# Performance work log

Hardware: AMD Instinct MI355X
Metric: run time of the kernel (lower is better)

## Reference

```python
import jax, jax.numpy as jnp
import numpy as np

B, S_NEW, D = 8, 16, 2048
H, HD = 16, 128
PAST = 4096


def setup_inputs() -> dict:
    key = jax.random.key(0)
    ks = jax.random.split(key, 8)
    w = 0.02
    return {
        "x": jax.random.normal(ks[0], (B, S_NEW, D), jnp.float32),
        "k_cache": jax.random.normal(ks[1], (B, H, PAST, HD), jnp.float32),
        "v_cache": jax.random.normal(ks[2], (B, H, PAST, HD), jnp.float32),
        "Wq": jax.random.normal(ks[3], (D, D), jnp.float32) * w,
        "bq": jnp.zeros((D,), jnp.float32),
        "Wk": jax.random.normal(ks[4], (D, D), jnp.float32) * w,
        "bk": jnp.zeros((D,), jnp.float32),
        "Wv": jax.random.normal(ks[5], (D, D), jnp.float32) * w,
        "bv": jnp.zeros((D,), jnp.float32),
        "Wo": jax.random.normal(ks[6], (D, D), jnp.float32) * w,
        "bo": jnp.zeros((D,), jnp.float32),
    }


def reference(x, k_cache, v_cache, Wq, bq, Wk, bk, Wv, bv, Wo, bo):
    B_, S_new, D_ = x.shape
    H_ = H
    hd = D_ // H_
    scale = hd ** (-0.5)

    def proj(W, b):
        # [B,S,D] -> [B,H,S,hd]
        return (x @ W + b).reshape(B_, S_new, H_, hd).transpose(0, 2, 1, 3)

    q = proj(Wq, bq)
    k_new = proj(Wk, bk)
    v_new = proj(Wv, bv)

    # cache.append + get_full_kv: concat along sequence axis
    k = jnp.concatenate([k_cache, k_new], axis=2)  # [B,H,S_full,hd]
    v = jnp.concatenate([v_cache, v_new], axis=2)
    S_full = k.shape[2]
    past = S_full - S_new

    scores = jnp.einsum("bhqd,bhkd->bhqk", q, k) * scale  # [B,H,S_new,S_full]

    # triu(ones(S_new,S_full), diagonal=past+1): mask key j when j - i > past
    i = jnp.arange(S_new)[:, None]
    j = jnp.arange(S_full)[None, :]
    mask = (j - i) > past  # [S_new, S_full] bool
    scores = jnp.where(mask[None, None, :, :], -jnp.inf, scores)

    attn = jax.nn.softmax(scores, axis=-1)  # dropout is identity in eval
    out = jnp.einsum("bhqk,bhkd->bhqd", attn, v)  # [B,H,S_new,hd]
    out = out.transpose(0, 2, 1, 3).reshape(B_, S_new, D_)
    return out @ Wo + bo
```

## Files before the change

kernel.cpp:

```cpp
#include <hip/hip_runtime.h>
#include <stdint.h>

#define B_    8
#define SNEW  16
#define D_    2048
#define H_    16
#define HD_   128
#define PAST_ 4096
#define LOG2E 1.4426950408889634f
#define SCALE 0.08838834764831845f
#define QSCALE (SCALE * LOG2E)

#define NCHUNK 16

#define KSTRIDE 136
#define VSTRIDE 18

typedef __attribute__((ext_vector_type(8))) short bf16x8;
typedef __attribute__((ext_vector_type(4))) float f32x4;

union BF8 { bf16x8 v; unsigned int u[4]; unsigned short s[8]; };

__device__ __forceinline__ unsigned int pk2(float a, float b) {
  unsigned int r;
  asm("v_cvt_pk_bf16_f32 %0, %1, %2" : "=v"(r) : "v"(a), "v"(b));
  return r;
}

__global__ __launch_bounds__(256) void k_cvt_x(const float* __restrict__ x,
                                               unsigned short* __restrict__ xb) {
  int i = blockIdx.x * 256 + threadIdx.x;
  const float4* xs = (const float4*)x;
  float4 a = xs[i * 2], b = xs[i * 2 + 1];
  uint4 v;
  v.x = pk2(a.x, a.y); v.y = pk2(a.z, a.w);
  v.z = pk2(b.x, b.y); v.w = pk2(b.z, b.w);
  ((uint4*)xb)[i] = v;
}

__global__ __launch_bounds__(256) void k_qkv(
    const unsigned short* __restrict__ xb,
    const float* __restrict__ Wq, const float* __restrict__ bq,
    const float* __restrict__ Wk, const float* __restrict__ bk,
    const float* __restrict__ Wv, const float* __restrict__ bv,
    unsigned short* __restrict__ qb, unsigned short* __restrict__ kbn,
    unsigned short* __restrict__ vbn) {
  __shared__ float red[4][128][16];
  const int n0g = blockIdx.x * 16;
  const int mat = n0g >> 11;
  const int n0 = n0g & 2047;
  const float* W    = (mat == 0) ? Wq : ((mat == 1) ? Wk : Wv);
  const float* bias = (mat == 0) ? bq : ((mat == 1) ? bk : bv);
  const int tid = threadIdx.x, w = tid >> 6, lane = tid & 63;
  const int nl = lane & 15, g = lane >> 4;

  f32x4 acc[8];
#pragma unroll
  for (int i = 0; i < 8; i++) acc[i] = (f32x4){0.f, 0.f, 0.f, 0.f};

  const int k0w = w * 512;
  float bw[8];
#pragma unroll
  for (int j = 0; j < 8; j++) bw[j] = W[(size_t)(k0w + g * 8 + j) * 2048 + n0 + nl];

  for (int kc = 0; kc < 16; kc++) {
    const int kbase = k0w + kc * 32 + g * 8;
    float nbw[8];
    if (kc < 15) {
#pragma unroll
      for (int j = 0; j < 8; j++) nbw[j] = W[(size_t)(kbase + 32 + j) * 2048 + n0 + nl];
    }
    BF8 bf;
#pragma unroll
    for (int j2 = 0; j2 < 4; j2++) bf.u[j2] = pk2(bw[2 * j2], bw[2 * j2 + 1]);
#pragma unroll
    for (int mt = 0; mt < 8; mt++) {
      bf16x8 a = *(const bf16x8*)(xb + (size_t)(mt * 16 + nl) * 2048 + kbase);
      acc[mt] = __builtin_amdgcn_mfma_f32_16x16x32_bf16(a, bf.v, acc[mt], 0, 0, 0);
    }
    if (kc < 15) {
#pragma unroll
      for (int j = 0; j < 8; j++) bw[j] = nbw[j];
    }
  }
#pragma unroll
  for (int mt = 0; mt < 8; mt++) {
    red[w][mt * 16 + g * 4 + 0][nl] = acc[mt][0];
    red[w][mt * 16 + g * 4 + 1][nl] = acc[mt][1];
    red[w][mt * 16 + g * 4 + 2][nl] = acc[mt][2];
    red[w][mt * 16 + g * 4 + 3][nl] = acc[mt][3];
  }
  __syncthreads();
  const int m = tid >> 1;
  const int c0 = (tid & 1) * 8;
  float sv[8];
#pragma unroll
  for (int i = 0; i < 8; i++)
    sv[i] = red[0][m][c0 + i] + red[1][m][c0 + i] + red[2][m][c0 + i] +
            red[3][m][c0 + i] + bias[n0 + c0 + i];
  const int bb = m >> 4, srow = m & 15;
  const int nglob = n0 + c0;
  const int hh = nglob >> 7, dd = nglob & 127;
  size_t ob = (((size_t)(bb * H_ + hh) * SNEW + srow) * HD_ + dd);
  uint4 v;
  if (mat == 0) {
    v.x = pk2(sv[0] * QSCALE, sv[1] * QSCALE); v.y = pk2(sv[2] * QSCALE, sv[3] * QSCALE);
    v.z = pk2(sv[4] * QSCALE, sv[5] * QSCALE); v.w = pk2(sv[6] * QSCALE, sv[7] * QSCALE);
    *(uint4*)(qb + ob) = v;
  } else {
    v.x = pk2(sv[0], sv[1]); v.y = pk2(sv[2], sv[3]);
    v.z = pk2(sv[4], sv[5]); v.w = pk2(sv[6], sv[7]);
    if (mat == 1) *(uint4*)(kbn + ob) = v;
    else          *(uint4*)(vbn + ob) = v;
  }
}

__global__ __launch_bounds__(256, 3) void k_attn(
    const float* __restrict__ kcache, const float* __restrict__ vcache,
    const unsigned short* __restrict__ qb, const unsigned short* __restrict__ kbn,
    const unsigned short* __restrict__ vbn,
    float* __restrict__ pO, float* __restrict__ pml) {
  __shared__ char smem[40960];
  unsigned short* Klds = (unsigned short*)smem;
  unsigned short* Vlds = (unsigned short*)(smem + 17408);
  unsigned short* QP   = (unsigned short*)(smem + 35840);
  float* cO  = (float*)smem;
  float* cml = (float*)(smem + 32768);

  const int chunk = blockIdx.x;
  const int h = blockIdx.y, b = blockIdx.z;
  const int bh = b * H_ + h;
  const int tid = threadIdx.x;
  const int w = tid >> 6, lane = tid & 63;
  const int nl = lane & 15, g = lane >> 4;

  const int CK = PAST_ / NCHUNK;
  const int key0 = chunk * CK + w * (CK / 4);
  const int NIT = CK / 4 / 16;
  const bool lastw = (chunk == NCHUNK - 1) && (w == 3);
  const int itend = NIT + (lastw ? 1 : 0);

  const float4* kbase = (const float4*)(kcache + ((size_t)bh * PAST_ + key0) * HD_);
  const float4* vbase = (const float4*)(vcache + ((size_t)bh * PAST_ + key0) * HD_);

  float4 kreg[8], vreg[8];
#pragma unroll
  for (int i = 0; i < 8; i++) kreg[i] = kbase[lane + i * 64];
#pragma unroll
  for (int i = 0; i < 8; i++) vreg[i] = vbase[lane + i * 64];

  {
    uint4 v = ((const uint4*)(qb + (size_t)bh * 2048))[tid];
    int e = tid * 8;
    *(uint4*)(QP + (e >> 7) * KSTRIDE + (e & 127)) = v;
  }
  __syncthreads();
  bf16x8 qfrag[4];
#pragma unroll
  for (int kc4 = 0; kc4 < 4; kc4++)
    qfrag[kc4] = *(const bf16x8*)(QP + nl * KSTRIDE + kc4 * 32 + g * 8);
  __syncthreads();
  for (int i = tid; i < 1280; i += 256) ((unsigned int*)QP)[i] = 0u;
  __syncthreads();

  unsigned short* Kw = Klds + w * (16 * KSTRIDE);
  unsigned short* Vw = Vlds + w * (128 * VSTRIDE);
  unsigned short* Pw = QP + w * (16 * 40);

  f32x4 Oacc[8];
#pragma unroll
  for (int i = 0; i < 8; i++) Oacc[i] = (f32x4){0.f, 0.f, 0.f, 0.f};
  float m_run = -1e30f, l_run = 0.f;

  for (int it = 0; it < itend; it++) {
    if (it < NIT) {
#pragma unroll
      for (int i = 0; i < 8; i++) {
        float4 kv = kreg[i];
        int e = (lane + i * 64) * 4;
        uint2 p; p.x = pk2(kv.x, kv.y); p.y = pk2(kv.z, kv.w);
        *(uint2*)(Kw + (e >> 7) * KSTRIDE + (e & 127)) = p;
      }
#pragma unroll
      for (int i = 0; i < 8; i++) {
        float4 vv = vreg[i];
        int idx = lane + i * 64;
        int r = idx >> 5;
        int d0 = (idx & 31) * 4;
        unsigned int c01 = pk2(vv.x, vv.y);
        unsigned int c23 = pk2(vv.z, vv.w);
        int rs = r ^ (((d0 >> 5) & 1) << 3);
        Vw[(d0 + 0) * VSTRIDE + rs] = (unsigned short)c01;
        Vw[(d0 + 1) * VSTRIDE + rs] = (unsigned short)(c01 >> 16);
        Vw[(d0 + 2) * VSTRIDE + rs] = (unsigned short)c23;
        Vw[(d0 + 3) * VSTRIDE + rs] = (unsigned short)(c23 >> 16);
      }
      if (it + 1 < NIT) {
        const float4* kn = kbase + (size_t)(it + 1) * 512;
        const float4* vn = vbase + (size_t)(it + 1) * 512;
#pragma unroll
        for (int i = 0; i < 8; i++) kreg[i] = kn[lane + i * 64];
#pragma unroll
        for (int i = 0; i < 8; i++) vreg[i] = vn[lane + i * 64];
      }
    } else {
      const uint4* ks = (const uint4*)(kbn + (size_t)bh * 2048);
      const uint4* vs = (const uint4*)(vbn + (size_t)bh * 2048);
#pragma unroll
      for (int i = 0; i < 4; i++) {
        uint4 v = ks[lane + i * 64];
        int e = (lane + i * 64) * 8;
        *(uint4*)(Kw + (e >> 7) * KSTRIDE + (e & 127)) = v;
      }
#pragma unroll
      for (int i = 0; i < 4; i++) {
        uint4 v2 = vs[lane + i * 64];
        int idx = lane + i * 64;
        int r = idx >> 4;
        int d0 = (idx & 15) * 8;
        int rs = r ^ (((d0 >> 5) & 1) << 3);
        unsigned int uu[4] = {v2.x, v2.y, v2.z, v2.w};
#pragma unroll
        for (int j2 = 0; j2 < 4; j2++) {
          Vw[(d0 + 2 * j2 + 0) * VSTRIDE + rs] = (unsigned short)uu[j2];
          Vw[(d0 + 2 * j2 + 1) * VSTRIDE + rs] = (unsigned short)(uu[j2] >> 16);
        }
      }
    }

    f32x4 sacc = (f32x4){0.f, 0.f, 0.f, 0.f};
#pragma unroll
    for (int kc4 = 0; kc4 < 4; kc4++) {
      bf16x8 a = *(const bf16x8*)(Kw + nl * KSTRIDE + kc4 * 32 + g * 8);
      sacc = __builtin_amdgcn_mfma_f32_16x16x32_bf16(a, qfrag[kc4], sacc, 0, 0, 0);
    }
    float s0 = sacc[0], s1 = sacc[1], s2 = sacc[2], s3 = sacc[3];
    if (it == NIT) {
      if (g * 4 + 0 > nl) s0 = -1e30f;
      if (g * 4 + 1 > nl) s1 = -1e30f;
      if (g * 4 + 2 > nl) s2 = -1e30f;
      if (g * 4 + 3 > nl) s3 = -1e30f;
    }
    float kmax = fmaxf(fmaxf(s0, s1), fmaxf(s2, s3));
    kmax = fmaxf(kmax, __shfl_xor(kmax, 16, 64));
    kmax = fmaxf(kmax, __shfl_xor(kmax, 32, 64));
    float newm = fmaxf(m_run, kmax);
    float p0 = exp2f(s0 - newm), p1 = exp2f(s1 - newm);
    float p2 = exp2f(s2 - newm), p3 = exp2f(s3 - newm);
    float psum = p0 + p1 + p2 + p3;
    psum += __shfl_xor(psum, 16, 64);
    psum += __shfl_xor(psum, 32, 64);
    float alpha = exp2f(m_run - newm);
    l_run = l_run * alpha + psum;
    m_run = newm;
    float ar0 = __shfl(alpha, g * 4 + 0, 64);
    float ar1 = __shfl(alpha, g * 4 + 1, 64);
    float ar2 = __shfl(alpha, g * 4 + 2, 64);
    float ar3 = __shfl(alpha, g * 4 + 3, 64);
#pragma unroll
    for (int nt = 0; nt < 8; nt++) {
      Oacc[nt][0] *= ar0; Oacc[nt][1] *= ar1;
      Oacc[nt][2] *= ar2; Oacc[nt][3] *= ar3;
    }
    *(unsigned int*)(Pw + nl * 40 + g * 4)     = pk2(p0, p1);
    *(unsigned int*)(Pw + nl * 40 + g * 4 + 2) = pk2(p2, p3);
    bf16x8 pfrag = *(const bf16x8*)(Pw + nl * 40 + g * 8);
#pragma unroll
    for (int nt = 0; nt < 8; nt++) {
      int row = nt * 16 + nl;
      const unsigned int* vp = (const unsigned int*)(
          Vw + row * VSTRIDE + (((g & 1) << 3) ^ ((nt & 2) << 2)));
      BF8 vb;
      vb.u[0] = vp[0]; vb.u[1] = vp[1]; vb.u[2] = vp[2]; vb.u[3] = vp[3];
      Oacc[nt] = __builtin_amdgcn_mfma_f32_16x16x32_bf16(pfrag, vb.v, Oacc[nt], 0, 0, 0);
    }
  }

  __syncthreads();
  float* cOw = cO + w * (16 * 128);
#pragma unroll
  for (int nt = 0; nt < 8; nt++) {
    cOw[(g * 4 + 0) * 128 + nt * 16 + nl] = Oacc[nt][0];
    cOw[(g * 4 + 1) * 128 + nt * 16 + nl] = Oacc[nt][1];
    cOw[(g * 4 + 2) * 128 + nt * 16 + nl] = Oacc[nt][2];
    cOw[(g * 4 + 3) * 128 + nt * 16 + nl] = Oacc[nt][3];
  }
  if (g == 0) { cml[(w * 16 + nl) * 2] = m_run; cml[(w * 16 + nl) * 2 + 1] = l_run; }
  __syncthreads();

  const int q = tid >> 4;
  const int d0 = (tid & 15) * 8;
  float M = -1e30f, mws[4], lws[4];
#pragma unroll
  for (int ww = 0; ww < 4; ww++) {
    mws[ww] = cml[(ww * 16 + q) * 2];
    lws[ww] = cml[(ww * 16 + q) * 2 + 1];
    M = fmaxf(M, mws[ww]);
  }
  float L = 0.f, o[8];
#pragma unroll
  for (int i = 0; i < 8; i++) o[i] = 0.f;
#pragma unroll
  for (int ww = 0; ww < 4; ww++) {
    float Wt = exp2f(mws[ww] - M);
    L += Wt * lws[ww];
    const float* src = cO + ww * 2048 + q * 128 + d0;
#pragma unroll
    for (int i = 0; i < 8; i++) o[i] += Wt * src[i];
  }
  size_t pb = (((size_t)bh * NCHUNK + chunk) * 16 + q) * 128 + d0;
  float4 st0 = {o[0], o[1], o[2], o[3]}, st1 = {o[4], o[5], o[6], o[7]};
  *(float4*)(pO + pb) = st0;
  *(float4*)(pO + pb + 4) = st1;
  if ((tid & 15) == 0) {
    size_t mb = (((size_t)bh * NCHUNK + chunk) * 16 + q) * 2;
    pml[mb] = M; pml[mb + 1] = L;
  }
}

__global__ __launch_bounds__(256) void k_comb(const float* __restrict__ pO,
                                              const float* __restrict__ pml,
                                              float* __restrict__ attn) {
  const int bh = blockIdx.x, tid = threadIdx.x;
  const int q = tid >> 4, d0 = (tid & 15) * 8;
  float M = -1e30f, mc[NCHUNK], lc[NCHUNK];
#pragma unroll
  for (int c = 0; c < NCHUNK; c++) {
    size_t mb = (((size_t)bh * NCHUNK + c) * 16 + q) * 2;
    mc[c] = pml[mb]; lc[c] = pml[mb + 1];
    M = fmaxf(M, mc[c]);
  }
  float L = 0.f, o[8];
#pragma unroll
  for (int i = 0; i < 8; i++) o[i] = 0.f;
#pragma unroll
  for (int c = 0; c < NCHUNK; c++) {
    float Wt = exp2f(mc[c] - M);
    L += Wt * lc[c];
    const float* src = pO + (((size_t)bh * NCHUNK + c) * 16 + q) * 128 + d0;
#pragma unroll
    for (int i = 0; i < 8; i++) o[i] += Wt * src[i];
  }
  float inv = 1.f / L;
  int b = bh >> 4, h = bh & 15;
  float* dst = attn + ((size_t)(b * SNEW + q)) * D_ + h * HD_ + d0;
  float4 s0 = {o[0] * inv, o[1] * inv, o[2] * inv, o[3] * inv};
  float4 s1 = {o[4] * inv, o[5] * inv, o[6] * inv, o[7] * inv};
  *(float4*)dst = s0;
  *(float4*)(dst + 4) = s1;
}

__global__ __launch_bounds__(256) void k_oproj(const float* __restrict__ attn,
                                               const float* __restrict__ Wo,
                                               const float* __restrict__ bo,
                                               float* __restrict__ out) {
  __shared__ float red[4][128][16];
  const int n0 = blockIdx.x * 16;
  const int tid = threadIdx.x, w = tid >> 6, lane = tid & 63;
  const int nl = lane & 15, g = lane >> 4;
  f32x4 acc[8];
#pragma unroll
  for (int i = 0; i < 8; i++) acc[i] = (f32x4){0.f, 0.f, 0.f, 0.f};
  const int k0w = w * 512;
  float bw[8];
#pragma unroll
  for (int j = 0; j < 8; j++) bw[j] = Wo[(size_t)(k0w + g * 8 + j) * 2048 + n0 + nl];
  for (int kc = 0; kc < 16; kc++) {
    const int kbase = k0w + kc * 32 + g * 8;
    float nbw[8];
    if (kc < 15) {
#pragma unroll
      for (int j = 0; j < 8; j++) nbw[j] = Wo[(size_t)(kbase + 32 + j) * 2048 + n0 + nl];
    }
    BF8 bf;
#pragma unroll
    for (int j2 = 0; j2 < 4; j2++) bf.u[j2] = pk2(bw[2 * j2], bw[2 * j2 + 1]);
#pragma unroll
    for (int mt = 0; mt < 8; mt++) {
      const float* ap = attn + (size_t)(mt * 16 + nl) * 2048 + kbase;
      float4 a0 = *(const float4*)ap;
      float4 a1 = *(const float4*)(ap + 4);
      BF8 af;
      af.u[0] = pk2(a0.x, a0.y); af.u[1] = pk2(a0.z, a0.w);
      af.u[2] = pk2(a1.x, a1.y); af.u[3] = pk2(a1.z, a1.w);
      acc[mt] = __builtin_amdgcn_mfma_f32_16x16x32_bf16(af.v, bf.v, acc[mt], 0, 0, 0);
    }
    if (kc < 15) {
#pragma unroll
      for (int j = 0; j < 8; j++) bw[j] = nbw[j];
    }
  }
#pragma unroll
  for (int mt = 0; mt < 8; mt++) {
    red[w][mt * 16 + g * 4 + 0][nl] = acc[mt][0];
    red[w][mt * 16 + g * 4 + 1][nl] = acc[mt][1];
    red[w][mt * 16 + g * 4 + 2][nl] = acc[mt][2];
    red[w][mt * 16 + g * 4 + 3][nl] = acc[mt][3];
  }
  __syncthreads();
  const int m = tid >> 1;
  const int c0 = (tid & 1) * 8;
  float sv[8];
#pragma unroll
  for (int i = 0; i < 8; i++)
    sv[i] = red[0][m][c0 + i] + red[1][m][c0 + i] + red[2][m][c0 + i] +
            red[3][m][c0 + i] + bo[n0 + c0 + i];
  float* dst = out + (size_t)m * 2048 + n0 + c0;
  float4 s0 = {sv[0], sv[1], sv[2], sv[3]}, s1 = {sv[4], sv[5], sv[6], sv[7]};
  *(float4*)dst = s0;
  *(float4*)(dst + 4) = s1;
}

extern "C" void kernel_launch(void* const* d_in, const int* in_sizes, int n_in,
                              void* d_out, int out_size, void* d_ws, size_t ws_size,
                              hipStream_t stream) {
  const float* x  = (const float*)d_in[0];
  const float* kc = (const float*)d_in[1];
  const float* vc = (const float*)d_in[2];
  const float* Wq = (const float*)d_in[3];
  const float* bq = (const float*)d_in[4];
  const float* Wk = (const float*)d_in[5];
  const float* bk = (const float*)d_in[6];
  const float* Wv = (const float*)d_in[7];
  const float* bv = (const float*)d_in[8];
  const float* Wo = (const float*)d_in[9];
  const float* bo = (const float*)d_in[10];
  float* out = (float*)d_out;

  char* ws = (char*)d_ws;
  unsigned short* xb   = (unsigned short*)(ws + 0);
  unsigned short* qb   = (unsigned short*)(ws + 524288);
  unsigned short* kbn  = (unsigned short*)(ws + 1048576);
  unsigned short* vbn  = (unsigned short*)(ws + 1572864);
  float*          attn = (float*)(ws + 2097152);
  float*          pO   = (float*)(ws + 3145728);
  float*          pml  = (float*)(ws + 19922944);

  k_cvt_x<<<128, 256, 0, stream>>>(x, xb);
  k_qkv<<<384, 256, 0, stream>>>(xb, Wq, bq, Wk, bk, Wv, bv, qb, kbn, vbn);
  k_attn<<<dim3(NCHUNK, H_, B_), 256, 0, stream>>>(kc, vc, qb, kbn, vbn, pO, pml);
  k_comb<<<B_ * H_, 256, 0, stream>>>(pO, pml, attn);
  k_oproj<<<128, 256, 0, stream>>>(attn, Wo, bo, out);
}
```

Measured before the change: 665.6 us.

## Restructure attention into single-wave blocks with async global-to-LDS double buffering

The attention kernel now runs one 64-lane wave per block and streams fp32 K/V tiles straight into LDS with global_load_lds, double-buffered and gated by vmcnt waits. The per-thread register staging and the bf16 conversion before the LDS store are removed, and K uses an XOR-swizzled layout. Conversion to bf16 now happens on LDS reads. The new-token block is handled in a separate tail, and the in-block four-wave merge is dropped. The aim is to overlap HBM loads with MFMA work and cut register and sync overhead. The cost is fp32 tiles doubling LDS traffic, scalar strided V reads with conversion, and fewer waves per block to hide latency.

New measurement: 652.5 us. 1.02x faster.

```diff
diff --git a/kernel.cpp b/kernel.cpp
--- a/kernel.cpp
+++ b/kernel.cpp
@@ -13,9 +13,6 @@
 
 #define NCHUNK 16
 
-#define KSTRIDE 136
-#define VSTRIDE 18
-
 typedef __attribute__((ext_vector_type(8))) short bf16x8;
 typedef __attribute__((ext_vector_type(4))) float f32x4;
 
@@ -25,6 +22,12 @@
   unsigned int r;
   asm("v_cvt_pk_bf16_f32 %0, %1, %2" : "=v"(r) : "v"(a), "v"(b));
   return r;
+}
+
+typedef __attribute__((address_space(1))) const unsigned int* as1cu;
+typedef __attribute__((address_space(3))) unsigned int* as3u;
+__device__ __forceinline__ void gl_lds16(const void* g, void* l) {
+  __builtin_amdgcn_global_load_lds((as1cu)g, (as3u)l, 16, 0, 0);
 }
 
 __global__ __launch_bounds__(256) void k_cvt_x(const float* __restrict__ x,
@@ -115,132 +118,86 @@
   }
 }
 
-__global__ __launch_bounds__(256, 3) void k_attn(
+__global__ __launch_bounds__(64) void k_attn(
     const float* __restrict__ kcache, const float* __restrict__ vcache,
     const unsigned short* __restrict__ qb, const unsigned short* __restrict__ kbn,
     const unsigned short* __restrict__ vbn,
     float* __restrict__ pO, float* __restrict__ pml) {
-  __shared__ char smem[40960];
-  unsigned short* Klds = (unsigned short*)smem;
-  unsigned short* Vlds = (unsigned short*)(smem + 17408);
-  unsigned short* QP   = (unsigned short*)(smem + 35840);
-  float* cO  = (float*)smem;
-  float* cml = (float*)(smem + 32768);
+  __shared__ __align__(16) char smem[34048];
 
   const int chunk = blockIdx.x;
   const int h = blockIdx.y, b = blockIdx.z;
   const int bh = b * H_ + h;
-  const int tid = threadIdx.x;
-  const int w = tid >> 6, lane = tid & 63;
+  const int lane = threadIdx.x & 63;
   const int nl = lane & 15, g = lane >> 4;
 
-  const int CK = PAST_ / NCHUNK;
-  const int key0 = chunk * CK + w * (CK / 4);
-  const int NIT = CK / 4 / 16;
-  const bool lastw = (chunk == NCHUNK - 1) && (w == 3);
-  const int itend = NIT + (lastw ? 1 : 0);
-
-  const float4* kbase = (const float4*)(kcache + ((size_t)bh * PAST_ + key0) * HD_);
-  const float4* vbase = (const float4*)(vcache + ((size_t)bh * PAST_ + key0) * HD_);
-
-  float4 kreg[8], vreg[8];
-#pragma unroll
-  for (int i = 0; i < 8; i++) kreg[i] = kbase[lane + i * 64];
-#pragma unroll
-  for (int i = 0; i < 8; i++) vreg[i] = vbase[lane + i * 64];
-
+  unsigned short* Pw = (unsigned short*)(smem + 32768);
+#pragma unroll
+  for (int i = 0; i < 5; i++) ((unsigned int*)Pw)[lane + i * 64] = 0u;
+
+  int koff[8];
   {
-    uint4 v = ((const uint4*)(qb + (size_t)bh * 2048))[tid];
-    int e = tid * 8;
-    *(uint4*)(QP + (e >> 7) * KSTRIDE + (e & 127)) = v;
-  }
-  __syncthreads();
+    int rl = lane >> 5, s5 = lane & 31;
+#pragma unroll
+    for (int i = 0; i < 8; i++) {
+      int r = 2 * i + rl;
+      koff[i] = r * 512 + ((s5 ^ (r & 7)) << 4);
+    }
+  }
+
   bf16x8 qfrag[4];
 #pragma unroll
   for (int kc4 = 0; kc4 < 4; kc4++)
-    qfrag[kc4] = *(const bf16x8*)(QP + nl * KSTRIDE + kc4 * 32 + g * 8);
-  __syncthreads();
-  for (int i = tid; i < 1280; i += 256) ((unsigned int*)QP)[i] = 0u;
-  __syncthreads();
-
-  unsigned short* Kw = Klds + w * (16 * KSTRIDE);
-  unsigned short* Vw = Vlds + w * (128 * VSTRIDE);
-  unsigned short* Pw = QP + w * (16 * 40);
+    qfrag[kc4] = *(const bf16x8*)(qb + (size_t)bh * 2048 + nl * 128 + kc4 * 32 + g * 8);
+  asm volatile("s_waitcnt vmcnt(0)" ::: "memory");
+  __builtin_amdgcn_sched_barrier(0);
+
+  const char* kt = (const char*)kcache + (size_t)(bh * PAST_ + chunk * 256) * 512;
+  const char* vt = (const char*)vcache + (size_t)(bh * PAST_ + chunk * 256) * 512;
+
+#pragma unroll
+  for (int i = 0; i < 8; i++) gl_lds16(kt + koff[i], smem + i * 1024);
+#pragma unroll
+  for (int i = 0; i < 8; i++) gl_lds16(vt + i * 1024 + lane * 16, smem + 16384 + i * 1024);
 
   f32x4 Oacc[8];
 #pragma unroll
   for (int i = 0; i < 8; i++) Oacc[i] = (f32x4){0.f, 0.f, 0.f, 0.f};
   float m_run = -1e30f, l_run = 0.f;
 
-  for (int it = 0; it < itend; it++) {
-    if (it < NIT) {
-#pragma unroll
-      for (int i = 0; i < 8; i++) {
-        float4 kv = kreg[i];
-        int e = (lane + i * 64) * 4;
-        uint2 p; p.x = pk2(kv.x, kv.y); p.y = pk2(kv.z, kv.w);
-        *(uint2*)(Kw + (e >> 7) * KSTRIDE + (e & 127)) = p;
-      }
-#pragma unroll
-      for (int i = 0; i < 8; i++) {
-        float4 vv = vreg[i];
-        int idx = lane + i * 64;
-        int r = idx >> 5;
-        int d0 = (idx & 31) * 4;
-        unsigned int c01 = pk2(vv.x, vv.y);
-        unsigned int c23 = pk2(vv.z, vv.w);
-        int rs = r ^ (((d0 >> 5) & 1) << 3);
-        Vw[(d0 + 0) * VSTRIDE + rs] = (unsigned short)c01;
-        Vw[(d0 + 1) * VSTRIDE + rs] = (unsigned short)(c01 >> 16);
-        Vw[(d0 + 2) * VSTRIDE + rs] = (unsigned short)c23;
-        Vw[(d0 + 3) * VSTRIDE + rs] = (unsigned short)(c23 >> 16);
-      }
-      if (it + 1 < NIT) {
-        const float4* kn = kbase + (size_t)(it + 1) * 512;
-        const float4* vn = vbase + (size_t)(it + 1) * 512;
-#pragma unroll
-        for (int i = 0; i < 8; i++) kreg[i] = kn[lane + i * 64];
-#pragma unroll
-        for (int i = 0; i < 8; i++) vreg[i] = vn[lane + i * 64];
-      }
+  for (int t = 0; t < 16; t++) {
+    if (t < 15) {
+      const char* ktn = kt + (size_t)(t + 1) * 8192;
+      const char* vtn = vt + (size_t)(t + 1) * 8192;
+      char* kb   = smem + ((t + 1) & 1) * 8192;
+      char* vbuf = smem + 16384 + ((t + 1) & 1) * 8192;
+#pragma unroll
+      for (int i = 0; i < 8; i++) gl_lds16(ktn + koff[i], kb + i * 1024);
+#pragma unroll
+      for (int i = 0; i < 8; i++) gl_lds16(vtn + i * 1024 + lane * 16, vbuf + i * 1024);
+      asm volatile("s_waitcnt vmcnt(16)" ::: "memory");
     } else {
-      const uint4* ks = (const uint4*)(kbn + (size_t)bh * 2048);
-      const uint4* vs = (const uint4*)(vbn + (size_t)bh * 2048);
-#pragma unroll
-      for (int i = 0; i < 4; i++) {
-        uint4 v = ks[lane + i * 64];
-        int e = (lane + i * 64) * 8;
-        *(uint4*)(Kw + (e >> 7) * KSTRIDE + (e & 127)) = v;
-      }
-#pragma unroll
-      for (int i = 0; i < 4; i++) {
-        uint4 v2 = vs[lane + i * 64];
-        int idx = lane + i * 64;
-        int r = idx >> 4;
-        int d0 = (idx & 15) * 8;
-        int rs = r ^ (((d0 >> 5) & 1) << 3);
-        unsigned int uu[4] = {v2.x, v2.y, v2.z, v2.w};
-#pragma unroll
-        for (int j2 = 0; j2 < 4; j2++) {
-          Vw[(d0 + 2 * j2 + 0) * VSTRIDE + rs] = (unsigned short)uu[j2];
-          Vw[(d0 + 2 * j2 + 1) * VSTRIDE + rs] = (unsigned short)(uu[j2] >> 16);
-        }
-      }
-    }
+      asm volatile("s_waitcnt vmcnt(0)" ::: "memory");
+    }
+    __builtin_amdgcn_sched_barrier(0);
+
+    const char*  Kb = smem + (t & 1) * 8192;
+    const float* Vb = (const float*)(smem + 16384 + (t & 1) * 8192);
 
     f32x4 sacc = (f32x4){0.f, 0.f, 0.f, 0.f};
 #pragma unroll
     for (int kc4 = 0; kc4 < 4; kc4++) {
-      bf16x8 a = *(const bf16x8*)(Kw + nl * KSTRIDE + kc4 * 32 + g * 8);
-      sacc = __builtin_amdgcn_mfma_f32_16x16x32_bf16(a, qfrag[kc4], sacc, 0, 0, 0);
-    }
+      int c0 = kc4 * 8 + g * 2;
+      int s0i = ((c0 ^ (nl & 7)) << 4), s1i = (((c0 + 1) ^ (nl & 7)) << 4);
+      f32x4 a0 = *(const f32x4*)(Kb + nl * 512 + s0i);
+      f32x4 a1 = *(const f32x4*)(Kb + nl * 512 + s1i);
+      BF8 af;
+      af.u[0] = pk2(a0[0], a0[1]); af.u[1] = pk2(a0[2], a0[3]);
+      af.u[2] = pk2(a1[0], a1[1]); af.u[3] = pk2(a1[2], a1[3]);
+      sacc = __builtin_amdgcn_mfma_f32_16x16x32_bf16(af.v, qfrag[kc4], sacc, 0, 0, 0);
+    }
+
     float s0 = sacc[0], s1 = sacc[1], s2 = sacc[2], s3 = sacc[3];
-    if (it == NIT) {
-      if (g * 4 + 0 > nl) s0 = -1e30f;
-      if (g * 4 + 1 > nl) s1 = -1e30f;
-      if (g * 4 + 2 > nl) s2 = -1e30f;
-      if (g * 4 + 3 > nl) s3 = -1e30f;
-    }
     float kmax = fmaxf(fmaxf(s0, s1), fmaxf(s2, s3));
     kmax = fmaxf(kmax, __shfl_xor(kmax, 16, 64));
     kmax = fmaxf(kmax, __shfl_xor(kmax, 32, 64));
@@ -265,19 +222,72 @@
     *(unsigned int*)(Pw + nl * 40 + g * 4)     = pk2(p0, p1);
     *(unsigned int*)(Pw + nl * 40 + g * 4 + 2) = pk2(p2, p3);
     bf16x8 pfrag = *(const bf16x8*)(Pw + nl * 40 + g * 8);
+
 #pragma unroll
     for (int nt = 0; nt < 8; nt++) {
-      int row = nt * 16 + nl;
-      const unsigned int* vp = (const unsigned int*)(
-          Vw + row * VSTRIDE + (((g & 1) << 3) ^ ((nt & 2) << 2)));
       BF8 vb;
-      vb.u[0] = vp[0]; vb.u[1] = vp[1]; vb.u[2] = vp[2]; vb.u[3] = vp[3];
+#pragma unroll
+      for (int j2 = 0; j2 < 4; j2++) {
+        int r0 = (g * 8 + 2 * j2) & 15, r1 = (g * 8 + 2 * j2 + 1) & 15;
+        vb.u[j2] = pk2(Vb[r0 * 128 + nt * 16 + nl], Vb[r1 * 128 + nt * 16 + nl]);
+      }
       Oacc[nt] = __builtin_amdgcn_mfma_f32_16x16x32_bf16(pfrag, vb.v, Oacc[nt], 0, 0, 0);
     }
   }
 
-  __syncthreads();
-  float* cOw = cO + w * (16 * 128);
+  if (chunk == NCHUNK - 1) {
+    const unsigned short* kb_ = kbn + (size_t)bh * 2048;
+    const unsigned short* vb_ = vbn + (size_t)bh * 2048;
+    f32x4 sacc = (f32x4){0.f, 0.f, 0.f, 0.f};
+#pragma unroll
+    for (int kc4 = 0; kc4 < 4; kc4++) {
+      bf16x8 a = *(const bf16x8*)(kb_ + nl * 128 + kc4 * 32 + g * 8);
+      sacc = __builtin_amdgcn_mfma_f32_16x16x32_bf16(a, qfrag[kc4], sacc, 0, 0, 0);
+    }
+    float s0 = sacc[0], s1 = sacc[1], s2 = sacc[2], s3 = sacc[3];
+    if (g * 4 + 0 > nl) s0 = -1e30f;
+    if (g * 4 + 1 > nl) s1 = -1e30f;
+    if (g * 4 + 2 > nl) s2 = -1e30f;
+    if (g * 4 + 3 > nl) s3 = -1e30f;
+    float kmax = fmaxf(fmaxf(s0, s1), fmaxf(s2, s3));
+    kmax = fmaxf(kmax, __shfl_xor(kmax, 16, 64));
+    kmax = fmaxf(kmax, __shfl_xor(kmax, 32, 64));
+    float newm = fmaxf(m_run, kmax);
+    float p0 = exp2f(s0 - newm), p1 = exp2f(s1 - newm);
+    float p2 = exp2f(s2 - newm), p3 = exp2f(s3 - newm);
+    float psum = p0 + p1 + p2 + p3;
+    psum += __shfl_xor(psum, 16, 64);
+    psum += __shfl_xor(psum, 32, 64);
+    float alpha = exp2f(m_run - newm);
+    l_run = l_run * alpha + psum;
+    m_run = newm;
+    float ar0 = __shfl(alpha, g * 4 + 0, 64);
+    float ar1 = __shfl(alpha, g * 4 + 1, 64);
+    float ar2 = __shfl(alpha, g * 4 + 2, 64);
+    float ar3 = __shfl(alpha, g * 4 + 3, 64);
+#pragma unroll
+    for (int nt = 0; nt < 8; nt++) {
+      Oacc[nt][0] *= ar0; Oacc[nt][1] *= ar1;
+      Oacc[nt][2] *= ar2; Oacc[nt][3] *= ar3;
+    }
+    *(unsigned int*)(Pw + nl * 40 + g * 4)     = pk2(p0, p1);
+    *(unsigned int*)(Pw + nl * 40 + g * 4 + 2) = pk2(p2, p3);
+    bf16x8 pfrag = *(const bf16x8*)(Pw + nl * 40 + g * 8);
+#pragma unroll
+    for (int nt = 0; nt < 8; nt++) {
+      BF8 vb;
+#pragma unroll
+      for (int j2 = 0; j2 < 4; j2++) {
+        int r0 = (g * 8 + 2 * j2) & 15, r1 = (g * 8 + 2 * j2 + 1) & 15;
+        unsigned int lo = vb_[r0 * 128 + nt * 16 + nl];
+        unsigned int hi = vb_[r1 * 128 + nt * 16 + nl];
+        vb.u[j2] = lo | (hi << 16);
+      }
+      Oacc[nt] = __builtin_amdgcn_mfma_f32_16x16x32_bf16(pfrag, vb.v, Oacc[nt], 0, 0, 0);
+    }
+  }
+
+  float* cOw = (float*)smem;
 #pragma unroll
   for (int nt = 0; nt < 8; nt++) {
     cOw[(g * 4 + 0) * 128 + nt * 16 + nl] = Oacc[nt][0];
@@ -285,36 +295,16 @@
     cOw[(g * 4 + 2) * 128 + nt * 16 + nl] = Oacc[nt][2];
     cOw[(g * 4 + 3) * 128 + nt * 16 + nl] = Oacc[nt][3];
   }
-  if (g == 0) { cml[(w * 16 + nl) * 2] = m_run; cml[(w * 16 + nl) * 2 + 1] = l_run; }
-  __syncthreads();
-
-  const int q = tid >> 4;
-  const int d0 = (tid & 15) * 8;
-  float M = -1e30f, mws[4], lws[4];
-#pragma unroll
-  for (int ww = 0; ww < 4; ww++) {
-    mws[ww] = cml[(ww * 16 + q) * 2];
-    lws[ww] = cml[(ww * 16 + q) * 2 + 1];
-    M = fmaxf(M, mws[ww]);
-  }
-  float L = 0.f, o[8];
-#pragma unroll
-  for (int i = 0; i < 8; i++) o[i] = 0.f;
-#pragma unroll
-  for (int ww = 0; ww < 4; ww++) {
-    float Wt = exp2f(mws[ww] - M);
-    L += Wt * lws[ww];
-    const float* src = cO + ww * 2048 + q * 128 + d0;
-#pragma unroll
-    for (int i = 0; i < 8; i++) o[i] += Wt * src[i];
-  }
-  size_t pb = (((size_t)bh * NCHUNK + chunk) * 16 + q) * 128 + d0;
-  float4 st0 = {o[0], o[1], o[2], o[3]}, st1 = {o[4], o[5], o[6], o[7]};
-  *(float4*)(pO + pb) = st0;
-  *(float4*)(pO + pb + 4) = st1;
-  if ((tid & 15) == 0) {
-    size_t mb = (((size_t)bh * NCHUNK + chunk) * 16 + q) * 2;
-    pml[mb] = M; pml[mb + 1] = L;
+  size_t pb = ((size_t)bh * NCHUNK + chunk) * 2048;
+#pragma unroll
+  for (int rr = 0; rr < 8; rr++) {
+    int f = lane + rr * 64;
+    float4 v = *(const float4*)(cOw + f * 4);
+    *(float4*)(pO + pb + f * 4) = v;
+  }
+  if (g == 0) {
+    size_t mb = (((size_t)bh * NCHUNK + chunk) * 16 + nl) * 2;
+    pml[mb] = m_run; pml[mb + 1] = l_run;
   }
 }
 
@@ -438,7 +428,7 @@
 
   k_cvt_x<<<128, 256, 0, stream>>>(x, xb);
   k_qkv<<<384, 256, 0, stream>>>(xb, Wq, bq, Wk, bk, Wv, bv, qb, kbn, vbn);
-  k_attn<<<dim3(NCHUNK, H_, B_), 256, 0, stream>>>(kc, vc, qb, kbn, vbn, pO, pml);
+  k_attn<<<dim3(NCHUNK, H_, B_), 64, 0, stream>>>(kc, vc, qb, kbn, vbn, pO, pml);
   k_comb<<<B_ * H_, 256, 0, stream>>>(pO, pml, attn);
   k_oproj<<<128, 256, 0, stream>>>(attn, Wo, bo, out);
 }
```
